# Kernel tuning notes

Measured on AMD Instinct MI355X. Metric: run time of the kernel, lower is better.

Reference implementation:

```python
import jax, jax.numpy as jnp
import numpy as np

B, N, DEG, D, ED = 4, 4096, 16, 128, 256
E = N * DEG
BN_EPS = 1e-5


def _l2norm(x):
    # F.normalize(p=2, dim=-1) with eps clamp
    n = jnp.linalg.norm(x, axis=-1, keepdims=True)
    return x / jnp.maximum(n, 1e-12)


def _bn_eval(x, g, b, m, v):
    return (x - m) * jax.lax.rsqrt(v + BN_EPS) * g + b


def setup_inputs() -> dict:
    key = jax.random.key(0)
    ks = jax.random.split(key, 8)
    node_feat = jax.random.normal(ks[0], (B, N, D), jnp.float32)
    # fixed-degree edge list, grouped by source node
    src_grp = jnp.broadcast_to(jnp.arange(N, dtype=jnp.int32)[:, None], (N, DEG))
    step = (N - 1) // DEG  # distinct targets per source
    tgt_grp = (src_grp + 1 + (jnp.arange(DEG, dtype=jnp.int32) * step)[None, :]) % N
    src_idx = jnp.broadcast_to(src_grp.reshape(1, E), (B, E)).astype(jnp.int32)
    tgt_grp_b = (tgt_grp[None] + jnp.arange(B, dtype=jnp.int32)[:, None, None]) % N
    tgt_idx = tgt_grp_b.reshape(B, E).astype(jnp.int32)

    def lin(k, fi, fo):
        return jax.random.normal(k, (fi, fo), jnp.float32) * (2.0 / fi) ** 0.5

    kk = jax.random.split(ks[1], 5)
    return {
        "node_feat": node_feat, "src_idx": src_idx, "tgt_idx": tgt_idx,
        "Wa1": lin(kk[0], 2 * D, D), "ba1": jnp.zeros((D,), jnp.float32),
        "Wa2": lin(kk[1], D, D), "ba2": jnp.zeros((D,), jnp.float32),
        "W1": lin(kk[2], 3 * D, ED), "b1": jnp.zeros((ED,), jnp.float32),
        "g1": jnp.ones((ED,), jnp.float32), "be1": jnp.zeros((ED,), jnp.float32),
        "m1": jnp.zeros((ED,), jnp.float32), "v1": jnp.ones((ED,), jnp.float32),
        "W2": lin(kk[3], ED, ED // 2), "b2": jnp.zeros((ED // 2,), jnp.float32),
        "g2": jnp.ones((ED // 2,), jnp.float32), "be2": jnp.zeros((ED // 2,), jnp.float32),
        "m2": jnp.zeros((ED // 2,), jnp.float32), "v2": jnp.ones((ED // 2,), jnp.float32),
        "W3": lin(kk[4], ED // 2, 1), "b3": jnp.zeros((1,), jnp.float32),
        "min_edges_per_node": 4,
    }


def reference(node_feat, src_idx, tgt_idx, Wa1, ba1, Wa2, ba2,
              W1, b1, g1, be1, m1, v1, W2, b2, g2, be2, m2, v2,
              W3, b3, min_edges_per_node):
    # gather endpoint features: [B, E, D]
    gather = jax.vmap(lambda nf, idx: nf[idx])
    sf = _l2norm(gather(node_feat, src_idx))
    tf = _l2norm(gather(node_feat, tgt_idx))
    feat_diff = jnp.abs(sf - tf)
    raw = jnp.concatenate([sf, tf], axis=-1)                      # [B,E,2D]
    att = jax.nn.softmax(jnp.maximum(raw @ Wa1 + ba1, 0.0) @ Wa2 + ba2, axis=-1)
    edge_feats = jnp.concatenate([sf, tf, feat_diff * att], axis=-1)  # [B,E,3D]
    h = jnp.maximum(_bn_eval(edge_feats @ W1 + b1, g1, be1, m1, v1), 0.0)
    h = jnp.maximum(_bn_eval(h @ W2 + b2, g2, be2, m2, v2), 0.0)
    logits = (h @ W3 + b3)[..., 0]                                # [B,E]
    scores = jax.nn.sigmoid(logits)

    # eval-mode 50th-percentile thresholding
    thr_idx = min(E * 50 // 100, E - 1)
    thr = jnp.sort(scores, axis=-1)[:, E - 1 - thr_idx]           # desc index thr_idx
    above = scores >= thr[:, None]
    # per-source repair of min_edges_per_node (edges grouped by src)
    grp_s = scores.reshape(B, N, DEG)
    grp_a = above.reshape(B, N, DEG)
    active = grp_a.sum(-1)
    me = jnp.int32(min_edges_per_node)
    need = jnp.where(active < me, jnp.minimum(me - active, DEG), 0)
    rank = jnp.argsort(jnp.argsort(-grp_s, axis=-1), axis=-1)     # 0 = highest score
    keep = grp_a | (rank < need[:, :, None])
    final = jnp.where(keep, grp_s, 0.0).reshape(B, E)

    # scatter to dense edge-weight matrix [B,N,N]
    b_ix = jnp.arange(B, dtype=jnp.int32)[:, None]
    edge_weights = jnp.zeros((B, N, N), final.dtype).at[b_ix, src_idx, tgt_idx].set(final)
    return edge_weights
```

## Files before the change

kernel.cpp:

```cpp
#include <hip/hip_runtime.h>
#include <math.h>

#define BB 4
#define NN 4096
#define DEGQ 16
#define DDIM 128
#define EDIM 256
#define EE (NN*DEGQ)

#define WS_XN     0
#define WS_UVPQ   (WS_XN + BB*NN*DDIM)
#define WS_SCORES (WS_UVPQ + (size_t)BB*NN*768)
#define WS_THR    (WS_SCORES + (size_t)BB*EE)
#define WS_SELP   (WS_THR + 8)
#define WS_SELR   (WS_SELP + 4)
#define WS_GHIST  (WS_SELR + 4)
#define WS_BN     (WS_GHIST + 1024)

__global__ void k_norm(const float* __restrict__ nf, float* __restrict__ xn) {
    int wave = (blockIdx.x * blockDim.x + threadIdx.x) >> 6;
    int lane = threadIdx.x & 63;
    if (wave >= BB * NN) return;
    const float* row = nf + (size_t)wave * DDIM;
    float2 v = *(const float2*)(row + 2 * lane);
    float ss = v.x * v.x + v.y * v.y;
#pragma unroll
    for (int d = 32; d; d >>= 1) ss += __shfl_xor(ss, d, 64);
    float n = fmaxf(sqrtf(ss), 1e-12f);
    float inv = 1.0f / n;
    float2 o; o.x = v.x * inv; o.y = v.y * inv;
    *(float2*)(xn + (size_t)wave * DDIM + 2 * lane) = o;
}

__global__ void k_prep(const float* g1, const float* be1, const float* m1, const float* v1,
                       const float* g2, const float* be2, const float* m2, const float* v2,
                       float* bn, unsigned* ghist, unsigned* selp, int* selr) {
    int c = threadIdx.x;
    ghist[c] = 0u; ghist[256 + c] = 0u; ghist[512 + c] = 0u; ghist[768 + c] = 0u;
    if (c < 4) { selp[c] = 0u; selr[c] = EE / 2 - 1; }
    if (c < 256) {
        float s = g1[c] / sqrtf(v1[c] + 1e-5f);
        bn[c] = s; bn[256 + c] = be1[c] - m1[c] * s;
    }
    if (c < 128) {
        float s = g2[c] / sqrtf(v2[c] + 1e-5f);
        bn[512 + c] = s; bn[640 + c] = be2[c] - m2[c] * s;
    }
}

__global__ void k_uvpq(const float* __restrict__ xn, const float* __restrict__ Wa1,
                       const float* __restrict__ W1, float* __restrict__ uvpq) {
    int chunk = blockIdx.y;
    const float* wbase; int wstride; int ocol;
    switch (chunk) {
        case 0: wbase = Wa1;                 wstride = 128; ocol = 0;   break;
        case 1: wbase = Wa1 + 128 * 128;     wstride = 128; ocol = 128; break;
        case 2: wbase = W1;                  wstride = 256; ocol = 256; break;
        case 3: wbase = W1 + 128;            wstride = 256; ocol = 384; break;
        case 4: wbase = W1 + 128 * 256;      wstride = 256; ocol = 512; break;
        default: wbase = W1 + 128 * 256 + 128; wstride = 256; ocol = 640; break;
    }
    int wv = threadIdx.x >> 6, lane = threadIdx.x & 63;
    int nodebase = blockIdx.x * 32 + wv * 8;
    const float* xrow[8];
#pragma unroll
    for (int j = 0; j < 8; ++j) xrow[j] = xn + (size_t)(nodebase + j) * DDIM;
    float acc0[8] = {}, acc1[8] = {};
#pragma unroll 4
    for (int k = 0; k < 128; ++k) {
        float w0 = wbase[k * wstride + lane];
        float w1 = wbase[k * wstride + 64 + lane];
#pragma unroll
        for (int j = 0; j < 8; ++j) {
            float a = xrow[j][k];
            acc0[j] = fmaf(a, w0, acc0[j]);
            acc1[j] = fmaf(a, w1, acc1[j]);
        }
    }
#pragma unroll
    for (int j = 0; j < 8; ++j) {
        float* orow = uvpq + (size_t)(nodebase + j) * 768 + ocol;
        orow[lane] = acc0[j];
        orow[64 + lane] = acc1[j];
    }
}

__global__ __launch_bounds__(512, 4) void
k_edge(const float* __restrict__ xn, const float* __restrict__ uvpq,
       const float* __restrict__ Wa2, const float* __restrict__ ba1,
       const float* __restrict__ ba2, const float* __restrict__ W1,
       const float* __restrict__ b1, const float* __restrict__ W2,
       const float* __restrict__ b2, const float* __restrict__ W3,
       const float* __restrict__ b3, const int* __restrict__ src,
       const int* __restrict__ tgt, const float* __restrict__ bn,
       float* __restrict__ scores) {
    __shared__ float act0[128 * 64];
    __shared__ float act1[128 * 64];
    __shared__ float pmax[8 * 64];
    __shared__ float pz[8 * 64];
    int tid = threadIdx.x;
    int lane = tid & 63;
    int wvs = (int)__builtin_amdgcn_readfirstlane(tid >> 6);
    int b = blockIdx.y;
    int T0 = blockIdx.x * 64;
    int se = src[(size_t)b * EE + T0 + lane];
    int te = tgt[(size_t)b * EE + T0 + lane];
    const float* uv = uvpq + (size_t)b * NN * 768;
    const float* xb = xn + (size_t)b * NN * DDIM;
    const float* up = uv + (size_t)se * 768;
    const float* vp = uv + (size_t)te * 768 + 128;
    int cb = wvs * 16;

#pragma unroll
    for (int q = 0; q < 4; ++q) {
        float4 uu = *(const float4*)(up + cb + 4 * q);
        float4 vv = *(const float4*)(vp + cb + 4 * q);
        float4 bv = *(const float4*)(ba1 + cb + 4 * q);
        act0[(cb + 4 * q + 0) * 64 + lane] = fmaxf(uu.x + vv.x + bv.x, 0.0f);
        act0[(cb + 4 * q + 1) * 64 + lane] = fmaxf(uu.y + vv.y + bv.y, 0.0f);
        act0[(cb + 4 * q + 2) * 64 + lane] = fmaxf(uu.z + vv.z + bv.z, 0.0f);
        act0[(cb + 4 * q + 3) * 64 + lane] = fmaxf(uu.w + vv.w + bv.w, 0.0f);
    }
    __syncthreads();

    float a[16] = {};
    {
        const float* wa = Wa2 + cb;
#pragma unroll 2
        for (int k = 0; k < 128; ++k) {
            float h = act0[k * 64 + lane];
            const float* wr = wa + k * 128;
#pragma unroll
            for (int i = 0; i < 16; ++i) a[i] = fmaf(h, wr[i], a[i]);
        }
#pragma unroll
        for (int i = 0; i < 16; ++i) a[i] += ba2[cb + i];
    }
    {
        float pm = a[0];
#pragma unroll
        for (int i = 1; i < 16; ++i) pm = fmaxf(pm, a[i]);
        pmax[wvs * 64 + lane] = pm;
    }
    __syncthreads();
    float m = pmax[lane];
#pragma unroll
    for (int w = 1; w < 8; ++w) m = fmaxf(m, pmax[w * 64 + lane]);
    float zp = 0.0f;
#pragma unroll
    for (int i = 0; i < 16; ++i) { a[i] = expf(a[i] - m); zp += a[i]; }
    pz[wvs * 64 + lane] = zp;
    __syncthreads();
    float z = pz[lane];
#pragma unroll
    for (int w = 1; w < 8; ++w) z += pz[w * 64 + lane];
    float inv = 1.0f / z;

#pragma unroll
    for (int q = 0; q < 4; ++q) {
        float4 xs = *(const float4*)(xb + (size_t)se * DDIM + cb + 4 * q);
        float4 xt = *(const float4*)(xb + (size_t)te * DDIM + cb + 4 * q);
        act0[(cb + 4 * q + 0) * 64 + lane] = fabsf(xs.x - xt.x) * a[4 * q + 0] * inv;
        act0[(cb + 4 * q + 1) * 64 + lane] = fabsf(xs.y - xt.y) * a[4 * q + 1] * inv;
        act0[(cb + 4 * q + 2) * 64 + lane] = fabsf(xs.z - xt.z) * a[4 * q + 2] * inv;
        act0[(cb + 4 * q + 3) * 64 + lane] = fabsf(xs.w - xt.w) * a[4 * q + 3] * inv;
    }
    __syncthreads();

    float acc[32] = {};
    {
        const float* wc = W1 + 256 * 256 + 2 * cb;
#pragma unroll 2
        for (int k = 0; k < 128; ++k) {
            float g = act0[k * 64 + lane];
            const float* wr = wc + k * 256;
#pragma unroll
            for (int i = 0; i < 32; ++i) acc[i] = fmaf(g, wr[i], acc[i]);
        }
    }
    {
        int cB = 2 * cb;
        const float* pr = uv + (size_t)se * 768 + 256 + cB;
        const float* qr = uv + (size_t)te * 768 + 512 + cB;
#pragma unroll
        for (int q = 0; q < 8; ++q) {
            float4 pv = *(const float4*)(pr + 4 * q);
            float4 qv = *(const float4*)(qr + 4 * q);
            float4 bv = *(const float4*)(b1 + cB + 4 * q);
            int c0 = cB + 4 * q;
            float y0 = acc[4 * q + 0] + pv.x + qv.x + bv.x;
            float y1 = acc[4 * q + 1] + pv.y + qv.y + bv.y;
            float y2 = acc[4 * q + 2] + pv.z + qv.z + bv.z;
            float y3 = acc[4 * q + 3] + pv.w + qv.w + bv.w;
            acc[4 * q + 0] = fmaxf(fmaf(y0, bn[c0 + 0], bn[256 + c0 + 0]), 0.0f);
            acc[4 * q + 1] = fmaxf(fmaf(y1, bn[c0 + 1], bn[256 + c0 + 1]), 0.0f);
            acc[4 * q + 2] = fmaxf(fmaf(y2, bn[c0 + 2], bn[256 + c0 + 2]), 0.0f);
            acc[4 * q + 3] = fmaxf(fmaf(y3, bn[c0 + 3], bn[256 + c0 + 3]), 0.0f);
        }
    }
    __syncthreads();
    {
        float* dst = (wvs < 4) ? act0 : act1;
        int rb = (wvs < 4) ? 2 * cb : 2 * cb - 128;
#pragma unroll
        for (int i = 0; i < 32; ++i) dst[(rb + i) * 64 + lane] = acc[i];
    }
    __syncthreads();

    float a3[16] = {};
    {
        const float* w2 = W2 + cb;
#pragma unroll 2
        for (int k = 0; k < 128; ++k) {
            float h = act0[k * 64 + lane];
            const float* wr = w2 + k * 128;
#pragma unroll
            for (int i = 0; i < 16; ++i) a3[i] = fmaf(h, wr[i], a3[i]);
        }
#pragma unroll 2
        for (int k = 0; k < 128; ++k) {
            float h = act1[k * 64 + lane];
            const float* wr = w2 + (k + 128) * 128;
#pragma unroll
            for (int i = 0; i < 16; ++i) a3[i] = fmaf(h, wr[i], a3[i]);
        }
    }
    float ps = 0.0f;
#pragma unroll
    for (int i = 0; i < 16; ++i) {
        int c = cb + i;
        float h3 = fmaxf(fmaf(a3[i] + b2[c], bn[512 + c], bn[640 + c]), 0.0f);
        ps += h3 * W3[c];
    }
    pmax[wvs * 64 + lane] = ps;
    __syncthreads();
    if (wvs == 0) {
        float lg = pmax[lane];
#pragma unroll
        for (int w = 1; w < 8; ++w) lg += pmax[w * 64 + lane];
        float sc = 1.0f / (1.0f + expf(-(lg + b3[0])));
        scores[(size_t)b * EE + T0 + lane] = sc;
    }
}

__global__ void k_hist(const float* __restrict__ scores, const unsigned* __restrict__ selp,
                       unsigned* __restrict__ ghist, int pass) {
    __shared__ unsigned h[256];
    int b = blockIdx.y;
    h[threadIdx.x] = 0u;
    __syncthreads();
    unsigned pref = selp[b];
    unsigned mask = (pass == 3) ? 0u : (0xFFFFFFFFu << ((pass + 1) * 8));
    const unsigned* sb = (const unsigned*)(scores + (size_t)b * EE);
    int base = blockIdx.x * 2048;
    for (int i = base + threadIdx.x; i < base + 2048; i += 256) {
        unsigned u = sb[i];
        if ((u & mask) == pref) atomicAdd(&h[(u >> (pass * 8)) & 255], 1u);
    }
    __syncthreads();
    unsigned v = h[threadIdx.x];
    if (v) atomicAdd(&ghist[b * 256 + threadIdx.x], v);
}

__global__ void k_pick(unsigned* __restrict__ ghist, unsigned* __restrict__ selp,
                       int* __restrict__ selr, float* __restrict__ thr, int pass) {
    __shared__ unsigned sh[256];
    int b = blockIdx.x;
    unsigned* gh = ghist + b * 256;
    sh[threadIdx.x] = gh[threadIdx.x];
    __syncthreads();
    if (threadIdx.x == 0) {
        unsigned r = (unsigned)selr[b], cum = 0;
        for (int x = 0; x < 256; ++x) {
            unsigned c = sh[x];
            if (cum + c > r) {
                selp[b] |= (unsigned)x << (pass * 8);
                selr[b] = (int)(r - cum);
                break;
            }
            cum += c;
        }
        if (pass == 0) thr[b] = __uint_as_float(selp[b]);
    }
    __syncthreads();
    gh[threadIdx.x] = 0u;
}

__global__ void k_scatter(const float* __restrict__ scores, const float* __restrict__ thr,
                          const int* __restrict__ src, const int* __restrict__ tgt,
                          const int* __restrict__ mep, float* __restrict__ out) {
    int gid = blockIdx.x * 256 + threadIdx.x;
    int b = gid >> 16;
    int lane = threadIdx.x & 63;
    int j = lane & 15;
    float s = scores[gid];
    float t = thr[b];
    bool above = (s >= t);
    unsigned long long bal = __ballot(above);
    int sub = lane >> 4;
    unsigned int mask16 = (unsigned int)((bal >> (sub * 16)) & 0xFFFFull);
    int active = __popc(mask16);
    int rank = 0;
#pragma unroll
    for (int j2 = 0; j2 < 16; ++j2) {
        float sv = __shfl(s, (lane & 48) + j2, 64);
        rank += (sv > s || (sv == s && j2 < j)) ? 1 : 0;
    }
    int me = *mep;
    int need = (active < me) ? min(me - active, DEGQ) : 0;
    bool keep = above || (rank < need);
    float wgt = keep ? s : 0.0f;
    out[(size_t)b * NN * NN + (size_t)src[gid] * NN + tgt[gid]] = wgt;
}

extern "C" void kernel_launch(void* const* d_in, const int* in_sizes, int n_in,
                              void* d_out, int out_size, void* d_ws, size_t ws_size,
                              hipStream_t stream) {
    const float* nf  = (const float*)d_in[0];
    const int*   src = (const int*)d_in[1];
    const int*   tgt = (const int*)d_in[2];
    const float* Wa1 = (const float*)d_in[3];
    const float* ba1 = (const float*)d_in[4];
    const float* Wa2 = (const float*)d_in[5];
    const float* ba2 = (const float*)d_in[6];
    const float* W1  = (const float*)d_in[7];
    const float* b1  = (const float*)d_in[8];
    const float* g1  = (const float*)d_in[9];
    const float* be1 = (const float*)d_in[10];
    const float* m1  = (const float*)d_in[11];
    const float* v1  = (const float*)d_in[12];
    const float* W2  = (const float*)d_in[13];
    const float* b2  = (const float*)d_in[14];
    const float* g2  = (const float*)d_in[15];
    const float* be2 = (const float*)d_in[16];
    const float* m2  = (const float*)d_in[17];
    const float* v2  = (const float*)d_in[18];
    const float* W3  = (const float*)d_in[19];
    const float* b3  = (const float*)d_in[20];
    const int*   mep = (const int*)d_in[21];

    float* ws = (float*)d_ws;
    float*    xn     = ws + WS_XN;
    float*    uvpq   = ws + WS_UVPQ;
    float*    scores = ws + WS_SCORES;
    float*    thrb   = ws + WS_THR;
    unsigned* selp   = (unsigned*)(ws + WS_SELP);
    int*      selr   = (int*)(ws + WS_SELR);
    unsigned* ghist  = (unsigned*)(ws + WS_GHIST);
    float*    bn     = ws + WS_BN;
    float*    out    = (float*)d_out;

    hipMemsetAsync(d_out, 0, (size_t)out_size * sizeof(float), stream);
    k_prep<<<1, 256, 0, stream>>>(g1, be1, m1, v1, g2, be2, m2, v2, bn, ghist, selp, selr);
    k_norm<<<(BB * NN) / 4, 256, 0, stream>>>(nf, xn);
    k_uvpq<<<dim3((BB * NN) / 32, 6), 256, 0, stream>>>(xn, Wa1, W1, uvpq);
    k_edge<<<dim3(EE / 64, BB), 512, 0, stream>>>(xn, uvpq, Wa2, ba1, ba2, W1, b1,
                                                  W2, b2, W3, b3, src, tgt, bn, scores);
    for (int pass = 3; pass >= 0; --pass) {
        k_hist<<<dim3(32, BB), 256, 0, stream>>>(scores, selp, ghist, pass);
        k_pick<<<BB, 256, 0, stream>>>(ghist, selp, selr, thrb, pass);
    }
    k_scatter<<<(BB * EE) / 256, 256, 0, stream>>>(scores, thrb, src, tgt, mep, out);
}
```

Baseline: 864.4 us.

## Register-tile edge MLP matmuls 4x4/4x8 per thread with padded shared layout

Replaces the one-edge-per-lane matmuls in the edge kernel, where every lane re-reads the same weight row, with a 2D register tiling. Each thread now computes 4 edges by 4 or 8 output columns, reading float4 activations from a shared buffer padded to stride 68 and float4 weight vectors. The goal is to cut weight-load traffic and LDS reads per FMA, raising arithmetic intensity. In exchange it adds more reduction partials (32 per edge for the final logit) and a larger shared pool, which may lower occupancy.

```diff
diff --git a/kernel.cpp b/kernel.cpp
--- a/kernel.cpp
+++ b/kernel.cpp
@@ -7,6 +7,7 @@
 #define DDIM 128
 #define EDIM 256
 #define EE (NN*DEGQ)
+#define S 68
 
 #define WS_XN     0
 #define WS_UVPQ   (WS_XN + BB*NN*DDIM)
@@ -94,10 +95,9 @@
        const float* __restrict__ b3, const int* __restrict__ src,
        const int* __restrict__ tgt, const float* __restrict__ bn,
        float* __restrict__ scores) {
-    __shared__ float act0[128 * 64];
-    __shared__ float act1[128 * 64];
-    __shared__ float pmax[8 * 64];
-    __shared__ float pz[8 * 64];
+    __shared__ float pool[256 * S];
+    __shared__ float red[2080];
+    __shared__ int ssrc[64], stgt[64];
     int tid = threadIdx.x;
     int lane = tid & 63;
     int wvs = (int)__builtin_amdgcn_readfirstlane(tid >> 6);
@@ -105,139 +105,194 @@
     int T0 = blockIdx.x * 64;
     int se = src[(size_t)b * EE + T0 + lane];
     int te = tgt[(size_t)b * EE + T0 + lane];
+    if (tid < 64) { ssrc[tid] = se; stgt[tid] = te; }
     const float* uv = uvpq + (size_t)b * NN * 768;
     const float* xb = xn + (size_t)b * NN * DDIM;
     const float* up = uv + (size_t)se * 768;
     const float* vp = uv + (size_t)te * 768 + 128;
     int cb = wvs * 16;
+    int wa = wvs & 1, wt = wvs >> 1;
+    int eg = lane >> 3, cg = lane & 7;
+    int e0 = 32 * wa + 4 * eg;
+    float* aT = pool + 128 * S;
 
 #pragma unroll
     for (int q = 0; q < 4; ++q) {
         float4 uu = *(const float4*)(up + cb + 4 * q);
         float4 vv = *(const float4*)(vp + cb + 4 * q);
         float4 bv = *(const float4*)(ba1 + cb + 4 * q);
-        act0[(cb + 4 * q + 0) * 64 + lane] = fmaxf(uu.x + vv.x + bv.x, 0.0f);
-        act0[(cb + 4 * q + 1) * 64 + lane] = fmaxf(uu.y + vv.y + bv.y, 0.0f);
-        act0[(cb + 4 * q + 2) * 64 + lane] = fmaxf(uu.z + vv.z + bv.z, 0.0f);
-        act0[(cb + 4 * q + 3) * 64 + lane] = fmaxf(uu.w + vv.w + bv.w, 0.0f);
-    }
-    __syncthreads();
-
-    float a[16] = {};
+        pool[(cb + 4 * q + 0) * S + lane] = fmaxf(uu.x + vv.x + bv.x, 0.0f);
+        pool[(cb + 4 * q + 1) * S + lane] = fmaxf(uu.y + vv.y + bv.y, 0.0f);
+        pool[(cb + 4 * q + 2) * S + lane] = fmaxf(uu.z + vv.z + bv.z, 0.0f);
+        pool[(cb + 4 * q + 3) * S + lane] = fmaxf(uu.w + vv.w + bv.w, 0.0f);
+    }
+    __syncthreads();
+
     {
-        const float* wa = Wa2 + cb;
+        int c0 = 32 * wt + 4 * cg;
+        const float* wp = Wa2 + c0;
+        float acc[4][4] = {};
+#pragma unroll 4
+        for (int k = 0; k < 128; ++k) {
+            float4 hv = *(const float4*)&pool[k * S + e0];
+            float4 wv = *(const float4*)(wp + k * 128);
+            acc[0][0] = fmaf(hv.x, wv.x, acc[0][0]); acc[0][1] = fmaf(hv.x, wv.y, acc[0][1]);
+            acc[0][2] = fmaf(hv.x, wv.z, acc[0][2]); acc[0][3] = fmaf(hv.x, wv.w, acc[0][3]);
+            acc[1][0] = fmaf(hv.y, wv.x, acc[1][0]); acc[1][1] = fmaf(hv.y, wv.y, acc[1][1]);
+            acc[1][2] = fmaf(hv.y, wv.z, acc[1][2]); acc[1][3] = fmaf(hv.y, wv.w, acc[1][3]);
+            acc[2][0] = fmaf(hv.z, wv.x, acc[2][0]); acc[2][1] = fmaf(hv.z, wv.y, acc[2][1]);
+            acc[2][2] = fmaf(hv.z, wv.z, acc[2][2]); acc[2][3] = fmaf(hv.z, wv.w, acc[2][3]);
+            acc[3][0] = fmaf(hv.w, wv.x, acc[3][0]); acc[3][1] = fmaf(hv.w, wv.y, acc[3][1]);
+            acc[3][2] = fmaf(hv.w, wv.z, acc[3][2]); acc[3][3] = fmaf(hv.w, wv.w, acc[3][3]);
+        }
+#pragma unroll
+        for (int j = 0; j < 4; ++j) {
+            float4 o; o.x = acc[0][j]; o.y = acc[1][j]; o.z = acc[2][j]; o.w = acc[3][j];
+            *(float4*)&aT[(c0 + j) * S + e0] = o;
+        }
+    }
+    __syncthreads();
+
+    {
+        float a[16];
+#pragma unroll
+        for (int i = 0; i < 16; ++i) a[i] = aT[(cb + i) * S + lane] + ba2[cb + i];
+        float pm = a[0];
+#pragma unroll
+        for (int i = 1; i < 16; ++i) pm = fmaxf(pm, a[i]);
+        red[wvs * 64 + lane] = pm;
+        __syncthreads();
+        float m = red[lane];
+#pragma unroll
+        for (int w = 1; w < 8; ++w) m = fmaxf(m, red[w * 64 + lane]);
+        float zp = 0.0f;
+#pragma unroll
+        for (int i = 0; i < 16; ++i) { a[i] = expf(a[i] - m); zp += a[i]; }
+        red[512 + wvs * 64 + lane] = zp;
+        __syncthreads();
+        float z = red[512 + lane];
+#pragma unroll
+        for (int w = 1; w < 8; ++w) z += red[512 + w * 64 + lane];
+        float inv = 1.0f / z;
+#pragma unroll
+        for (int q = 0; q < 4; ++q) {
+            float4 xs = *(const float4*)(xb + (size_t)se * DDIM + cb + 4 * q);
+            float4 xt = *(const float4*)(xb + (size_t)te * DDIM + cb + 4 * q);
+            pool[(cb + 4 * q + 0) * S + lane] = fabsf(xs.x - xt.x) * a[4 * q + 0] * inv;
+            pool[(cb + 4 * q + 1) * S + lane] = fabsf(xs.y - xt.y) * a[4 * q + 1] * inv;
+            pool[(cb + 4 * q + 2) * S + lane] = fabsf(xs.z - xt.z) * a[4 * q + 2] * inv;
+            pool[(cb + 4 * q + 3) * S + lane] = fabsf(xs.w - xt.w) * a[4 * q + 3] * inv;
+        }
+    }
+    __syncthreads();
+
+    {
+        int c0 = 64 * wt + 8 * cg;
+        const float* wp = W1 + 256 * 256 + c0;
+        float acc[4][8] = {};
 #pragma unroll 2
         for (int k = 0; k < 128; ++k) {
-            float h = act0[k * 64 + lane];
-            const float* wr = wa + k * 128;
-#pragma unroll
-            for (int i = 0; i < 16; ++i) a[i] = fmaf(h, wr[i], a[i]);
-        }
-#pragma unroll
-        for (int i = 0; i < 16; ++i) a[i] += ba2[cb + i];
-    }
+            float4 hv = *(const float4*)&pool[k * S + e0];
+            float4 w0 = *(const float4*)(wp + k * 256);
+            float4 w1 = *(const float4*)(wp + k * 256 + 4);
+            acc[0][0] = fmaf(hv.x, w0.x, acc[0][0]); acc[0][1] = fmaf(hv.x, w0.y, acc[0][1]);
+            acc[0][2] = fmaf(hv.x, w0.z, acc[0][2]); acc[0][3] = fmaf(hv.x, w0.w, acc[0][3]);
+            acc[0][4] = fmaf(hv.x, w1.x, acc[0][4]); acc[0][5] = fmaf(hv.x, w1.y, acc[0][5]);
+            acc[0][6] = fmaf(hv.x, w1.z, acc[0][6]); acc[0][7] = fmaf(hv.x, w1.w, acc[0][7]);
+            acc[1][0] = fmaf(hv.y, w0.x, acc[1][0]); acc[1][1] = fmaf(hv.y, w0.y, acc[1][1]);
+            acc[1][2] = fmaf(hv.y, w0.z, acc[1][2]); acc[1][3] = fmaf(hv.y, w0.w, acc[1][3]);
+            acc[1][4] = fmaf(hv.y, w1.x, acc[1][4]); acc[1][5] = fmaf(hv.y, w1.y, acc[1][5]);
+            acc[1][6] = fmaf(hv.y, w1.z, acc[1][6]); acc[1][7] = fmaf(hv.y, w1.w, acc[1][7]);
+            acc[2][0] = fmaf(hv.z, w0.x, acc[2][0]); acc[2][1] = fmaf(hv.z, w0.y, acc[2][1]);
+            acc[2][2] = fmaf(hv.z, w0.z, acc[2][2]); acc[2][3] = fmaf(hv.z, w0.w, acc[2][3]);
+            acc[2][4] = fmaf(hv.z, w1.x, acc[2][4]); acc[2][5] = fmaf(hv.z, w1.y, acc[2][5]);
+            acc[2][6] = fmaf(hv.z, w1.z, acc[2][6]); acc[2][7] = fmaf(hv.z, w1.w, acc[2][7]);
+            acc[3][0] = fmaf(hv.w, w0.x, acc[3][0]); acc[3][1] = fmaf(hv.w, w0.y, acc[3][1]);
+            acc[3][2] = fmaf(hv.w, w0.z, acc[3][2]); acc[3][3] = fmaf(hv.w, w0.w, acc[3][3]);
+            acc[3][4] = fmaf(hv.w, w1.x, acc[3][4]); acc[3][5] = fmaf(hv.w, w1.y, acc[3][5]);
+            acc[3][6] = fmaf(hv.w, w1.z, acc[3][6]); acc[3][7] = fmaf(hv.w, w1.w, acc[3][7]);
+        }
+        float4 bv0 = *(const float4*)(b1 + c0);
+        float4 bv1 = *(const float4*)(b1 + c0 + 4);
+        float4 s0 = *(const float4*)(bn + c0);
+        float4 s1 = *(const float4*)(bn + c0 + 4);
+        float4 t0 = *(const float4*)(bn + 256 + c0);
+        float4 t1 = *(const float4*)(bn + 256 + c0 + 4);
+#pragma unroll
+        for (int i = 0; i < 4; ++i) {
+            const float* pr = uv + (size_t)ssrc[e0 + i] * 768 + 256 + c0;
+            const float* qr = uv + (size_t)stgt[e0 + i] * 768 + 512 + c0;
+            float4 p0 = *(const float4*)(pr);
+            float4 p1 = *(const float4*)(pr + 4);
+            float4 q0 = *(const float4*)(qr);
+            float4 q1 = *(const float4*)(qr + 4);
+            float y0 = acc[i][0] + p0.x + q0.x + bv0.x;
+            float y1 = acc[i][1] + p0.y + q0.y + bv0.y;
+            float y2 = acc[i][2] + p0.z + q0.z + bv0.z;
+            float y3 = acc[i][3] + p0.w + q0.w + bv0.w;
+            float y4 = acc[i][4] + p1.x + q1.x + bv1.x;
+            float y5 = acc[i][5] + p1.y + q1.y + bv1.y;
+            float y6 = acc[i][6] + p1.z + q1.z + bv1.z;
+            float y7 = acc[i][7] + p1.w + q1.w + bv1.w;
+            acc[i][0] = fmaxf(fmaf(y0, s0.x, t0.x), 0.0f);
+            acc[i][1] = fmaxf(fmaf(y1, s0.y, t0.y), 0.0f);
+            acc[i][2] = fmaxf(fmaf(y2, s0.z, t0.z), 0.0f);
+            acc[i][3] = fmaxf(fmaf(y3, s0.w, t0.w), 0.0f);
+            acc[i][4] = fmaxf(fmaf(y4, s1.x, t1.x), 0.0f);
+            acc[i][5] = fmaxf(fmaf(y5, s1.y, t1.y), 0.0f);
+            acc[i][6] = fmaxf(fmaf(y6, s1.z, t1.z), 0.0f);
+            acc[i][7] = fmaxf(fmaf(y7, s1.w, t1.w), 0.0f);
+        }
+        __syncthreads();
+#pragma unroll
+        for (int j = 0; j < 8; ++j) {
+            float4 o; o.x = acc[0][j]; o.y = acc[1][j]; o.z = acc[2][j]; o.w = acc[3][j];
+            *(float4*)&pool[(c0 + j) * S + e0] = o;
+        }
+    }
+    __syncthreads();
+
     {
-        float pm = a[0];
-#pragma unroll
-        for (int i = 1; i < 16; ++i) pm = fmaxf(pm, a[i]);
-        pmax[wvs * 64 + lane] = pm;
-    }
-    __syncthreads();
-    float m = pmax[lane];
-#pragma unroll
-    for (int w = 1; w < 8; ++w) m = fmaxf(m, pmax[w * 64 + lane]);
-    float zp = 0.0f;
-#pragma unroll
-    for (int i = 0; i < 16; ++i) { a[i] = expf(a[i] - m); zp += a[i]; }
-    pz[wvs * 64 + lane] = zp;
-    __syncthreads();
-    float z = pz[lane];
-#pragma unroll
-    for (int w = 1; w < 8; ++w) z += pz[w * 64 + lane];
-    float inv = 1.0f / z;
-
-#pragma unroll
-    for (int q = 0; q < 4; ++q) {
-        float4 xs = *(const float4*)(xb + (size_t)se * DDIM + cb + 4 * q);
-        float4 xt = *(const float4*)(xb + (size_t)te * DDIM + cb + 4 * q);
-        act0[(cb + 4 * q + 0) * 64 + lane] = fabsf(xs.x - xt.x) * a[4 * q + 0] * inv;
-        act0[(cb + 4 * q + 1) * 64 + lane] = fabsf(xs.y - xt.y) * a[4 * q + 1] * inv;
-        act0[(cb + 4 * q + 2) * 64 + lane] = fabsf(xs.z - xt.z) * a[4 * q + 2] * inv;
-        act0[(cb + 4 * q + 3) * 64 + lane] = fabsf(xs.w - xt.w) * a[4 * q + 3] * inv;
-    }
-    __syncthreads();
-
-    float acc[32] = {};
-    {
-        const float* wc = W1 + 256 * 256 + 2 * cb;
-#pragma unroll 2
-        for (int k = 0; k < 128; ++k) {
-            float g = act0[k * 64 + lane];
-            const float* wr = wc + k * 256;
-#pragma unroll
-            for (int i = 0; i < 32; ++i) acc[i] = fmaf(g, wr[i], acc[i]);
-        }
-    }
-    {
-        int cB = 2 * cb;
-        const float* pr = uv + (size_t)se * 768 + 256 + cB;
-        const float* qr = uv + (size_t)te * 768 + 512 + cB;
-#pragma unroll
-        for (int q = 0; q < 8; ++q) {
-            float4 pv = *(const float4*)(pr + 4 * q);
-            float4 qv = *(const float4*)(qr + 4 * q);
-            float4 bv = *(const float4*)(b1 + cB + 4 * q);
-            int c0 = cB + 4 * q;
-            float y0 = acc[4 * q + 0] + pv.x + qv.x + bv.x;
-            float y1 = acc[4 * q + 1] + pv.y + qv.y + bv.y;
-            float y2 = acc[4 * q + 2] + pv.z + qv.z + bv.z;
-            float y3 = acc[4 * q + 3] + pv.w + qv.w + bv.w;
-            acc[4 * q + 0] = fmaxf(fmaf(y0, bn[c0 + 0], bn[256 + c0 + 0]), 0.0f);
-            acc[4 * q + 1] = fmaxf(fmaf(y1, bn[c0 + 1], bn[256 + c0 + 1]), 0.0f);
-            acc[4 * q + 2] = fmaxf(fmaf(y2, bn[c0 + 2], bn[256 + c0 + 2]), 0.0f);
-            acc[4 * q + 3] = fmaxf(fmaf(y3, bn[c0 + 3], bn[256 + c0 + 3]), 0.0f);
-        }
-    }
-    __syncthreads();
-    {
-        float* dst = (wvs < 4) ? act0 : act1;
-        int rb = (wvs < 4) ? 2 * cb : 2 * cb - 128;
-#pragma unroll
-        for (int i = 0; i < 32; ++i) dst[(rb + i) * 64 + lane] = acc[i];
-    }
-    __syncthreads();
-
-    float a3[16] = {};
-    {
-        const float* w2 = W2 + cb;
-#pragma unroll 2
-        for (int k = 0; k < 128; ++k) {
-            float h = act0[k * 64 + lane];
-            const float* wr = w2 + k * 128;
-#pragma unroll
-            for (int i = 0; i < 16; ++i) a3[i] = fmaf(h, wr[i], a3[i]);
-        }
-#pragma unroll 2
-        for (int k = 0; k < 128; ++k) {
-            float h = act1[k * 64 + lane];
-            const float* wr = w2 + (k + 128) * 128;
-#pragma unroll
-            for (int i = 0; i < 16; ++i) a3[i] = fmaf(h, wr[i], a3[i]);
-        }
-    }
-    float ps = 0.0f;
-#pragma unroll
-    for (int i = 0; i < 16; ++i) {
-        int c = cb + i;
-        float h3 = fmaxf(fmaf(a3[i] + b2[c], bn[512 + c], bn[640 + c]), 0.0f);
-        ps += h3 * W3[c];
-    }
-    pmax[wvs * 64 + lane] = ps;
-    __syncthreads();
+        int c0 = 32 * wt + 4 * cg;
+        const float* wp = W2 + c0;
+        float acc[4][4] = {};
+#pragma unroll 4
+        for (int k = 0; k < 256; ++k) {
+            float4 hv = *(const float4*)&pool[k * S + e0];
+            float4 wv = *(const float4*)(wp + k * 128);
+            acc[0][0] = fmaf(hv.x, wv.x, acc[0][0]); acc[0][1] = fmaf(hv.x, wv.y, acc[0][1]);
+            acc[0][2] = fmaf(hv.x, wv.z, acc[0][2]); acc[0][3] = fmaf(hv.x, wv.w, acc[0][3]);
+            acc[1][0] = fmaf(hv.y, wv.x, acc[1][0]); acc[1][1] = fmaf(hv.y, wv.y, acc[1][1]);
+            acc[1][2] = fmaf(hv.y, wv.z, acc[1][2]); acc[1][3] = fmaf(hv.y, wv.w, acc[1][3]);
+            acc[2][0] = fmaf(hv.z, wv.x, acc[2][0]); acc[2][1] = fmaf(hv.z, wv.y, acc[2][1]);
+            acc[2][2] = fmaf(hv.z, wv.z, acc[2][2]); acc[2][3] = fmaf(hv.z, wv.w, acc[2][3]);
+            acc[3][0] = fmaf(hv.w, wv.x, acc[3][0]); acc[3][1] = fmaf(hv.w, wv.y, acc[3][1]);
+            acc[3][2] = fmaf(hv.w, wv.z, acc[3][2]); acc[3][3] = fmaf(hv.w, wv.w, acc[3][3]);
+        }
+        float4 b2v = *(const float4*)(b2 + c0);
+        float4 s2v = *(const float4*)(bn + 512 + c0);
+        float4 t2v = *(const float4*)(bn + 640 + c0);
+        float4 w3v = *(const float4*)(W3 + c0);
+        int pidx = 8 * wt + cg;
+#pragma unroll
+        for (int i = 0; i < 4; ++i) {
+            float h0 = fmaxf(fmaf(acc[i][0] + b2v.x, s2v.x, t2v.x), 0.0f);
+            float h1 = fmaxf(fmaf(acc[i][1] + b2v.y, s2v.y, t2v.y), 0.0f);
+            float h2 = fmaxf(fmaf(acc[i][2] + b2v.z, s2v.z, t2v.z), 0.0f);
+            float h3 = fmaxf(fmaf(acc[i][3] + b2v.w, s2v.w, t2v.w), 0.0f);
+            float ps = h0 * w3v.x;
+            ps += h1 * w3v.y;
+            ps += h2 * w3v.z;
+            ps += h3 * w3v.w;
+            red[pidx * 65 + e0 + i] = ps;
+        }
+    }
+    __syncthreads();
+
     if (wvs == 0) {
-        float lg = pmax[lane];
-#pragma unroll
-        for (int w = 1; w < 8; ++w) lg += pmax[w * 64 + lane];
+        float lg = 0.0f;
+#pragma unroll
+        for (int p = 0; p < 32; ++p) lg += red[p * 65 + lane];
         float sc = 1.0f / (1.0f + expf(-(lg + b3[0])));
         scores[(size_t)b * EE + T0 + lane] = sc;
     }
```

New measurement: 903.4 us. 1.05x slower.
